# Kernel tuning notes

Measured on AMD Instinct MI355X. Metric: run time of the kernel, lower is better.

The kernel has to match this reference:

```python
import jax, jax.numpy as jnp
import numpy as np
import math

B, S, D = 4, 1024, 1024
H, DH = 16, 64
DFF = 4 * D
NEG = -1e9


def _layernorm(x, g, b, eps=1e-5):
    mu = jnp.mean(x, axis=-1, keepdims=True)
    var = jnp.var(x, axis=-1, keepdims=True)
    return (x - mu) * jax.lax.rsqrt(var + eps) * g + b


def setup_inputs() -> dict:
    key = jax.random.key(0)
    ks = jax.random.split(key, 12)
    inp = {
        "input": jax.random.normal(ks[0], (B, S, D), dtype=jnp.float32),
        # additive causal mask: 0 on/below diagonal, -1e9 above
        "causal_mask": jnp.where(
            jnp.tril(jnp.ones((S, S), dtype=bool)), 0.0, NEG
        ).astype(jnp.float32)[None, None],
        # additive padding mask: last 64 tokens of each sequence are padding
        "padding_mask": jnp.where(jnp.arange(S) < S - 64, 0.0, NEG)
        .astype(jnp.float32)[None, None, None, :]
        .repeat(B, axis=0),
        "ln1_g": jnp.ones((D,), jnp.float32), "ln1_b": jnp.zeros((D,), jnp.float32),
        "ln2_g": jnp.ones((D,), jnp.float32), "ln2_b": jnp.zeros((D,), jnp.float32),
        "ln3_g": jnp.ones((D,), jnp.float32), "ln3_b": jnp.zeros((D,), jnp.float32),
        "Wq": jax.random.normal(ks[1], (D, H * DH), jnp.float32) * 0.02,
        "bq": jnp.zeros((H * DH,), jnp.float32),
        "Wk": jax.random.normal(ks[2], (D, H * DH), jnp.float32) * 0.02,
        "bk": jnp.zeros((H * DH,), jnp.float32),
        "Wv": jax.random.normal(ks[3], (D, H * DH), jnp.float32) * 0.02,
        "bv": jnp.zeros((H * DH,), jnp.float32),
        "Wo": jax.random.normal(ks[4], (H * DH, D), jnp.float32) * 0.02,
        "bo": jnp.zeros((D,), jnp.float32),
        "W1": jax.random.normal(ks[5], (D, DFF), jnp.float32) * 0.02,
        "b1": jnp.zeros((DFF,), jnp.float32),
        "W2": jax.random.normal(ks[6], (DFF, D), jnp.float32) * 0.02,
        "b2": jnp.zeros((D,), jnp.float32),
    }
    return inp


def reference(input, causal_mask, padding_mask,
              ln1_g, ln1_b, ln2_g, ln2_b, ln3_g, ln3_b,
              Wq, bq, Wk, bk, Wv, bv, Wo, bo, W1, b1, W2, b2):
    x = _layernorm(input, ln1_g, ln1_b)
    b, s, _ = x.shape

    def heads(y):  # [b,s,H*DH] -> [b,H,s,DH]
        return y.reshape(b, s, H, DH).transpose(0, 2, 1, 3)

    q = heads(x @ Wq + bq)
    k = heads(x @ Wk + bk)
    v = heads(x @ Wv + bv)

    logits = jnp.einsum('bhqd,bhkd->bhqk', q, k) / math.sqrt(DH)
    logits = logits + causal_mask + padding_mask
    probs = jax.nn.softmax(logits, axis=-1)
    attn = jnp.einsum('bhqk,bhkd->bhqd', probs, v)
    attn = attn.transpose(0, 2, 1, 3).reshape(b, s, H * DH)  # b s (h d)
    attn_out = attn @ Wo + bo

    x = x + _layernorm(attn_out, ln2_g, ln2_b)
    h = _layernorm(x, ln3_g, ln3_b)
    x = x + (jax.nn.gelu(h @ W1 + b1, approximate=False) @ W2 + b2)
    return x
```

## Files before the change

### kernel.cpp

```cpp
#include <hip/hip_runtime.h>
#include <hip/hip_bf16.h>

typedef __hip_bfloat16 bf16;
typedef __bf16 bf16x8 __attribute__((ext_vector_type(8)));
typedef float f32x4 __attribute__((ext_vector_type(4)));

#define DEV __device__ __forceinline__

DEV int swz(int r, int k) { return r * 64 + (k ^ ((r & 7) << 3)); }

#define GLOAD_LDS16(gaddr, laddr)                                              \
  __builtin_amdgcn_global_load_lds(                                            \
      (const __attribute__((address_space(1))) void*)(gaddr),                  \
      (__attribute__((address_space(3))) void*)(laddr), 16, 0, 0)

__global__ void prep_kernel(
    const float* __restrict__ Wq, const float* __restrict__ Wk,
    const float* __restrict__ Wv, const float* __restrict__ Wo,
    const float* __restrict__ W1, const float* __restrict__ W2,
    const float* __restrict__ bq, const float* __restrict__ bk,
    const float* __restrict__ bv,
    bf16* __restrict__ WqkvT, bf16* __restrict__ WoT,
    bf16* __restrict__ W1T, bf16* __restrict__ W2T, float* __restrict__ bqkv) {
  int bid = blockIdx.x;
  if (bid >= 12288) {
    int i = (bid - 12288) * 256 + threadIdx.y * 32 + threadIdx.x;
    if (i < 3072)
      bqkv[i] = i < 1024 ? bq[i] : (i < 2048 ? bk[i - 1024] : bv[i - 2048]);
    return;
  }
  const float* src; bf16* dst; int K, N, tb;
  if (bid < 4096) {
    int wsel = bid >> 10;
    src = wsel == 0 ? Wq : wsel == 1 ? Wk : wsel == 2 ? Wv : Wo;
    dst = wsel < 3 ? WqkvT + (size_t)wsel * 1048576 : WoT;
    K = 1024; N = 1024; tb = bid & 1023;
  } else if (bid < 8192) {
    src = W1; dst = W1T; K = 1024; N = 4096; tb = bid - 4096;
  } else {
    src = W2; dst = W2T; K = 4096; N = 1024; tb = bid - 8192;
  }
  int ntx = N >> 5;
  int bx = (tb % ntx) * 32, by = (tb / ntx) * 32;
  __shared__ bf16 t[32][33];
  int tx = threadIdx.x, ty = threadIdx.y;
#pragma unroll
  for (int j = 0; j < 32; j += 8)
    t[ty + j][tx] = __float2bfloat16(src[(size_t)(by + ty + j) * N + bx + tx]);
  __syncthreads();
#pragma unroll
  for (int j = 0; j < 32; j += 8)
    dst[(size_t)(bx + ty + j) * K + by + tx] = t[tx][ty + j];
}

__global__ __launch_bounds__(256) void ln1_kernel(
    const float* __restrict__ in, const float* __restrict__ g, const float* __restrict__ b,
    float* __restrict__ xo, bf16* __restrict__ xb) {
  int row = blockIdx.x, tid = threadIdx.x;
  int lane = tid & 63, w = tid >> 6;
  float4 v = reinterpret_cast<const float4*>(in + (size_t)row * 1024)[tid];
  float s = v.x + v.y + v.z + v.w;
  float sq = v.x * v.x + v.y * v.y + v.z * v.z + v.w * v.w;
#pragma unroll
  for (int m = 32; m; m >>= 1) { s += __shfl_xor(s, m); sq += __shfl_xor(sq, m); }
  __shared__ float ss[4], qq[4];
  if (lane == 0) { ss[w] = s; qq[w] = sq; }
  __syncthreads();
  s = ss[0] + ss[1] + ss[2] + ss[3];
  sq = qq[0] + qq[1] + qq[2] + qq[3];
  float mu = s * (1.f / 1024.f);
  float rs = rsqrtf(sq * (1.f / 1024.f) - mu * mu + 1e-5f);
  float4 gg = reinterpret_cast<const float4*>(g)[tid];
  float4 bb = reinterpret_cast<const float4*>(b)[tid];
  float4 y;
  y.x = (v.x - mu) * rs * gg.x + bb.x;
  y.y = (v.y - mu) * rs * gg.y + bb.y;
  y.z = (v.z - mu) * rs * gg.z + bb.z;
  y.w = (v.w - mu) * rs * gg.w + bb.w;
  reinterpret_cast<float4*>(xo + (size_t)row * 1024)[tid] = y;
  union { bf16 h[4]; uint2 u; } pk;
  pk.h[0] = __float2bfloat16(y.x); pk.h[1] = __float2bfloat16(y.y);
  pk.h[2] = __float2bfloat16(y.z); pk.h[3] = __float2bfloat16(y.w);
  reinterpret_cast<uint2*>(xb + (size_t)row * 1024)[tid] = pk.u;
}

__global__ __launch_bounds__(256) void ln23_kernel(
    const float* __restrict__ x, const float* __restrict__ ao,
    const float* __restrict__ g2, const float* __restrict__ b2,
    const float* __restrict__ g3, const float* __restrict__ b3,
    float* __restrict__ x2o, bf16* __restrict__ hb) {
  int row = blockIdx.x, tid = threadIdx.x;
  int lane = tid & 63, w = tid >> 6;
  float4 a = reinterpret_cast<const float4*>(ao + (size_t)row * 1024)[tid];
  float s = a.x + a.y + a.z + a.w;
  float sq = a.x * a.x + a.y * a.y + a.z * a.z + a.w * a.w;
#pragma unroll
  for (int m = 32; m; m >>= 1) { s += __shfl_xor(s, m); sq += __shfl_xor(sq, m); }
  __shared__ float s1[4], q1[4], s2[4], q2[4];
  if (lane == 0) { s1[w] = s; q1[w] = sq; }
  __syncthreads();
  s = s1[0] + s1[1] + s1[2] + s1[3];
  sq = q1[0] + q1[1] + q1[2] + q1[3];
  float mu = s * (1.f / 1024.f);
  float rs = rsqrtf(sq * (1.f / 1024.f) - mu * mu + 1e-5f);
  float4 xr = reinterpret_cast<const float4*>(x + (size_t)row * 1024)[tid];
  float4 gg = reinterpret_cast<const float4*>(g2)[tid];
  float4 bb = reinterpret_cast<const float4*>(b2)[tid];
  float4 x2;
  x2.x = xr.x + (a.x - mu) * rs * gg.x + bb.x;
  x2.y = xr.y + (a.y - mu) * rs * gg.y + bb.y;
  x2.z = xr.z + (a.z - mu) * rs * gg.z + bb.z;
  x2.w = xr.w + (a.w - mu) * rs * gg.w + bb.w;
  reinterpret_cast<float4*>(x2o + (size_t)row * 1024)[tid] = x2;
  s = x2.x + x2.y + x2.z + x2.w;
  sq = x2.x * x2.x + x2.y * x2.y + x2.z * x2.z + x2.w * x2.w;
#pragma unroll
  for (int m = 32; m; m >>= 1) { s += __shfl_xor(s, m); sq += __shfl_xor(sq, m); }
  if (lane == 0) { s2[w] = s; q2[w] = sq; }
  __syncthreads();
  s = s2[0] + s2[1] + s2[2] + s2[3];
  sq = q2[0] + q2[1] + q2[2] + q2[3];
  mu = s * (1.f / 1024.f);
  rs = rsqrtf(sq * (1.f / 1024.f) - mu * mu + 1e-5f);
  gg = reinterpret_cast<const float4*>(g3)[tid];
  bb = reinterpret_cast<const float4*>(b3)[tid];
  union { bf16 h[4]; uint2 u; } pk;
  pk.h[0] = __float2bfloat16((x2.x - mu) * rs * gg.x + bb.x);
  pk.h[1] = __float2bfloat16((x2.y - mu) * rs * gg.y + bb.y);
  pk.h[2] = __float2bfloat16((x2.z - mu) * rs * gg.z + bb.z);
  pk.h[3] = __float2bfloat16((x2.w - mu) * rs * gg.w + bb.w);
  reinterpret_cast<uint2*>(hb + (size_t)row * 1024)[tid] = pk.u;
}

template <int BM, int BN, int WM, int WN, int MINW,
          bool GELU, bool RES, bool OUTBF, bool VSPLIT>
__global__ __launch_bounds__(WM * WN * 64, MINW) void gemm_db(
    const bf16* __restrict__ A, const bf16* __restrict__ BT,
    const float* __restrict__ bias, const float* __restrict__ res,
    float* __restrict__ outf, bf16* __restrict__ outb,
    bf16* __restrict__ kt, bf16* __restrict__ vt,
    int M, int N, int K) {
  constexpr int NW = WM * WN;
  constexpr int MT = BM / WM / 16, NT = BN / WN / 16;
  constexpr int ACH = BM / 8, BCH = BN / 8;
  constexpr int PW = (ACH + BCH) / NW;
  __shared__ __align__(16) bf16 As[2][BM * 64];
  __shared__ __align__(16) bf16 Bs[2][BN * 64];
  const int t = threadIdx.x, lane = t & 63, w = t >> 6;
  const int wr = w / WN, wc = w % WN;
  const int l15 = lane & 15, l4 = lane >> 4;
  const int gx = gridDim.x, nwg = gx * gridDim.y;
  int bid = blockIdx.y * gx + blockIdx.x;
  int sbid = (bid & 7) * (nwg >> 3) + (bid >> 3);
  const int m0 = (sbid / gx) * BM, n0 = (sbid % gx) * BN;
  const int lr = lane >> 3;
  const int scol = ((lane & 7) * 8) ^ (lr * 8);

  auto stage = [&](int buf, int kt_) {
    const int k0 = kt_ << 6;
#pragma unroll
    for (int i = 0; i < PW; ++i) {
      int c = w * PW + i;
      if (c < ACH) {
        GLOAD_LDS16(A + (size_t)(m0 + c * 8 + lr) * K + k0 + scol, &As[buf][c * 512]);
      } else {
        int c2 = c - ACH;
        GLOAD_LDS16(BT + (size_t)(n0 + c2 * 8 + lr) * K + k0 + scol, &Bs[buf][c2 * 512]);
      }
    }
  };

  f32x4 acc[MT][NT] = {};
  const int nk = K >> 6;
  stage(0, 0);
  __syncthreads();
  int cur = 0;
  for (int kk = 0; kk < nk; ++kk) {
    if (kk + 1 < nk) stage(cur ^ 1, kk + 1);
#pragma unroll
    for (int ks = 0; ks < 2; ++ks) {
      bf16x8 af[MT], bfr[NT];
#pragma unroll
      for (int m = 0; m < MT; ++m)
        af[m] = *reinterpret_cast<const bf16x8*>(
            &As[cur][swz(wr * (BM / WM) + m * 16 + l15, ks * 32 + l4 * 8)]);
#pragma unroll
      for (int n = 0; n < NT; ++n)
        bfr[n] = *reinterpret_cast<const bf16x8*>(
            &Bs[cur][swz(wc * (BN / WN) + n * 16 + l15, ks * 32 + l4 * 8)]);
      __builtin_amdgcn_s_setprio(1);
#pragma unroll
      for (int m = 0; m < MT; ++m)
#pragma unroll
        for (int n = 0; n < NT; ++n)
          acc[m][n] = __builtin_amdgcn_mfma_f32_16x16x32_bf16(af[m], bfr[n], acc[m][n], 0, 0, 0);
      __builtin_amdgcn_s_setprio(0);
    }
    __syncthreads();
    cur ^= 1;
  }

#pragma unroll
  for (int m = 0; m < MT; ++m) {
    int gr0 = m0 + wr * (BM / WM) + m * 16 + l4 * 4;
#pragma unroll
    for (int n = 0; n < NT; ++n) {
      int gc = n0 + wc * (BN / WN) + n * 16 + l15;
      float bv = bias[gc];
#pragma unroll
      for (int q = 0; q < 4; ++q) {
        int gr = gr0 + q;
        float v = acc[m][n][q] + bv;
        if constexpr (GELU) v = 0.5f * v * (1.f + erff(v * 0.70710678118654752f));
        if constexpr (RES) v += res[(size_t)gr * N + gc];
        if constexpr (VSPLIT) {
          int s = gr & 1023, bb = gr >> 10;
          if (gc < 1024) {
            outb[(size_t)gr * N + gc] = __float2bfloat16(v);
          } else if (gc < 2048) {
            int hd = gc - 1024, hh = hd >> 6, d = hd & 63;
            int ln = (s & 15) | (((d >> 3) & 3) << 4);
            kt[(((size_t)(bb * 16 + hh) * 64 + (s >> 4)) << 10) + (d >> 5) * 512 +
               ln * 8 + (d & 7)] = __float2bfloat16(v);
          } else {
            int hd = gc - 2048, hh = hd >> 6, d = hd & 63;
            int ln = (d & 15) | (((s >> 3) & 3) << 4);
            vt[(((size_t)(bb * 16 + hh) * 4 + (d >> 4)) << 14) + ((s >> 5) << 9) +
               ln * 8 + (s & 7)] = __float2bfloat16(v);
          }
        } else if constexpr (OUTBF) {
          outb[(size_t)gr * N + gc] = __float2bfloat16(v);
        } else {
          outf[(size_t)gr * N + gc] = v;
        }
      }
    }
  }
}

__global__ __launch_bounds__(256, 2) void attn_kernel(
    const bf16* __restrict__ qkv, const bf16* __restrict__ kt,
    const bf16* __restrict__ vt, bf16* __restrict__ o) {
  const int S = 1024, QS = 3072, HD = 1024;
  const bf16* qg = qkv;
  int bid = blockIdx.x;
  int xcd = bid & 7, j = bid >> 3;
  int grp = xcd * 8 + (j >> 3);
  int pr = j & 7;
  const int b = grp >> 4, h = grp & 15;
  const int t = threadIdx.x, lane = t & 63, w = t >> 6;
  const int l15 = lane & 15, l4 = lane >> 4;

  constexpr int PSTR = 72;
  __shared__ __align__(16) bf16 P[4][16 * PSTR];

  const int bh = b * 16 + h;
  const bf16* kbase = kt + ((size_t)bh << 16) + lane * 8;
  const bf16* vbase = vt + ((size_t)bh << 16) + lane * 8;

  bf16x8 kA[8], kB[8];
  auto loadK = [&](int kb, bf16x8* kf) {
#pragma unroll
    for (int cb = 0; cb < 4; ++cb)
#pragma unroll
      for (int ks = 0; ks < 2; ++ks)
        kf[cb * 2 + ks] = *reinterpret_cast<const bf16x8*>(
            kbase + (((kb >> 4) + cb) << 10) + (ks << 9));
  };

  auto run_strip = [&](int q0) {
    bf16x8 qf0, qf1;
    {
      const bf16* qp = qg + (size_t)(b * S + q0 + l15) * QS + h * 64 + l4 * 8;
      qf0 = *reinterpret_cast<const bf16x8*>(qp);
      qf1 = *reinterpret_cast<const bf16x8*>(qp + 32);
    }
    f32x4 acc[4] = {};
    float mrow = -1e30f, lrow = 0.f;
    const int kmaxa = q0 + 15, kmax = kmaxa < 959 ? kmaxa : 959;
    const int nt = (kmax >> 6) + 1;
    loadK(0, kA);

    for (int kt_ = 0; kt_ < nt; ++kt_) {
      const int kb = kt_ << 6;
      bf16x8* kf = (kt_ & 1) ? kB : kA;
      bf16x8* kn = (kt_ & 1) ? kA : kB;
      bf16x8 vf[8];
#pragma unroll
      for (int n = 0; n < 4; ++n)
#pragma unroll
        for (int ks = 0; ks < 2; ++ks)
          vf[n * 2 + ks] = *reinterpret_cast<const bf16x8*>(
              vbase + (n << 14) + (((kb >> 5) + ks) << 9));
      if (kt_ + 1 < nt) loadK(kb + 64, kn);

      f32x4 sc[4];
      __builtin_amdgcn_s_setprio(1);
#pragma unroll
      for (int cb = 0; cb < 4; ++cb) {
        f32x4 z = {};
        z = __builtin_amdgcn_mfma_f32_16x16x32_bf16(kf[cb * 2 + 0], qf0, z, 0, 0, 0);
        z = __builtin_amdgcn_mfma_f32_16x16x32_bf16(kf[cb * 2 + 1], qf1, z, 0, 0, 0);
        sc[cb] = z;
      }
      __builtin_amdgcn_s_setprio(0);

      const int q = q0 + l15;
      float p[16];
#pragma unroll
      for (int cb = 0; cb < 4; ++cb)
#pragma unroll
        for (int r = 0; r < 4; ++r) {
          int kgl = kb + cb * 16 + l4 * 4 + r;
          p[cb * 4 + r] = (kgl > q) ? -1e30f : sc[cb][r] * 0.125f;
        }
      float tm = p[0];
#pragma unroll
      for (int i = 1; i < 16; ++i) tm = fmaxf(tm, p[i]);
      tm = fmaxf(tm, __shfl_xor(tm, 16));
      tm = fmaxf(tm, __shfl_xor(tm, 32));
      bool defer = __all(tm <= mrow + 8.f);
      float mn = defer ? mrow : fmaxf(mrow, tm);
      float ps = 0.f;
#pragma unroll
      for (int i = 0; i < 16; ++i) { p[i] = __expf(p[i] - mn); ps += p[i]; }
      ps += __shfl_xor(ps, 16);
      ps += __shfl_xor(ps, 32);
      if (defer) {
        lrow += ps;
      } else {
        float al = __expf(mrow - mn);
        mrow = mn;
        lrow = lrow * al + ps;
#pragma unroll
        for (int n = 0; n < 4; ++n)
#pragma unroll
          for (int r = 0; r < 4; ++r) acc[n][r] *= al;
      }
#pragma unroll
      for (int cb = 0; cb < 4; ++cb) {
        union { bf16 h4[4]; uint2 u; } pk;
#pragma unroll
        for (int r = 0; r < 4; ++r) pk.h4[r] = __float2bfloat16(p[cb * 4 + r]);
        *reinterpret_cast<uint2*>(&P[w][l15 * PSTR + cb * 16 + l4 * 4]) = pk.u;
      }
      asm volatile("" ::: "memory");
      bf16x8 pb0 = *reinterpret_cast<const bf16x8*>(&P[w][l15 * PSTR + l4 * 8]);
      bf16x8 pb1 = *reinterpret_cast<const bf16x8*>(&P[w][l15 * PSTR + 32 + l4 * 8]);
      __builtin_amdgcn_s_setprio(1);
#pragma unroll
      for (int n = 0; n < 4; ++n) {
        acc[n] = __builtin_amdgcn_mfma_f32_16x16x32_bf16(vf[n * 2 + 0], pb0, acc[n], 0, 0, 0);
        acc[n] = __builtin_amdgcn_mfma_f32_16x16x32_bf16(vf[n * 2 + 1], pb1, acc[n], 0, 0, 0);
      }
      __builtin_amdgcn_s_setprio(0);
    }

    float inv = 1.f / lrow;
#pragma unroll
    for (int n = 0; n < 4; ++n) {
      union { bf16 h4[4]; uint2 u; } pk;
#pragma unroll
      for (int r = 0; r < 4; ++r) pk.h4[r] = __float2bfloat16(acc[n][r] * inv);
      *reinterpret_cast<uint2*>(&P[w][l15 * PSTR + n * 16 + l4 * 4]) = pk.u;
    }
    asm volatile("" ::: "memory");
    {
      int qq = lane >> 2, c = lane & 3;
#pragma unroll
      for (int i = 0; i < 2; ++i) {
        uint4 ov = *reinterpret_cast<const uint4*>(&P[w][qq * PSTR + c * 16 + i * 8]);
        *reinterpret_cast<uint4*>(
            o + (size_t)(b * S + q0 + qq) * HD + h * 64 + c * 16 + i * 8) = ov;
      }
    }
    asm volatile("" ::: "memory");
  };

  run_strip(pr * 64 + w * 16);
  run_strip((15 - pr) * 64 + w * 16);
}

extern "C" void kernel_launch(void* const* d_in, const int* in_sizes, int n_in,
                              void* d_out, int out_size, void* d_ws, size_t ws_size,
                              hipStream_t stream) {
  const float* input = (const float*)d_in[0];
  const float* ln1g = (const float*)d_in[3];
  const float* ln1b = (const float*)d_in[4];
  const float* ln2g = (const float*)d_in[5];
  const float* ln2b = (const float*)d_in[6];
  const float* ln3g = (const float*)d_in[7];
  const float* ln3b = (const float*)d_in[8];
  const float* Wq = (const float*)d_in[9];  const float* bq = (const float*)d_in[10];
  const float* Wk = (const float*)d_in[11]; const float* bk = (const float*)d_in[12];
  const float* Wv = (const float*)d_in[13]; const float* bv = (const float*)d_in[14];
  const float* Wo = (const float*)d_in[15]; const float* bo = (const float*)d_in[16];
  const float* W1 = (const float*)d_in[17]; const float* b1 = (const float*)d_in[18];
  const float* W2 = (const float*)d_in[19]; const float* b2 = (const float*)d_in[20];

  const int M = 4096, D = 1024, F = 4096;
  char* p = (char*)d_ws;
  size_t off = 0;
  auto nxt = [&](size_t n) { char* r = p + off; off += n; return r; };
  bf16* WqkvT = (bf16*)nxt((size_t)3 * D * D * 2);
  bf16* WoT = (bf16*)nxt((size_t)D * D * 2);
  bf16* W1T = (bf16*)nxt((size_t)F * D * 2);
  bf16* W2T = (bf16*)nxt((size_t)D * F * 2);
  float* bqkv = (float*)nxt(16384);
  float* xf  = (float*)nxt((size_t)M * D * 4);
  float* aof = (float*)nxt((size_t)M * D * 4);
  float* x2f = (float*)nxt((size_t)M * D * 4);
  bf16* xb = (bf16*)nxt((size_t)M * D * 2);
  bf16* qkv = (bf16*)nxt((size_t)M * 3 * D * 2);
  bf16* ktb = (bf16*)aof;
  bf16* vtb = (bf16*)((char*)aof + (size_t)8 * 1024 * 1024);
  bf16* gb = (bf16*)xf;
  bf16* ab = xb;
  bf16* hb = qkv;

  prep_kernel<<<12300, dim3(32, 8), 0, stream>>>(
      Wq, Wk, Wv, Wo, W1, W2, bq, bk, bv, WqkvT, WoT, W1T, W2T, bqkv);

  ln1_kernel<<<M, 256, 0, stream>>>(input, ln1g, ln1b, xf, xb);

  gemm_db<256, 256, 2, 4, 2, false, false, true, true>
      <<<dim3(12, 16), 512, 0, stream>>>(
      xb, WqkvT, bqkv, nullptr, nullptr, qkv, ktb, vtb, M, 3 * D, D);

  attn_kernel<<<512, 256, 0, stream>>>(qkv, ktb, vtb, ab);

  gemm_db<128, 64, 2, 2, 4, false, false, false, false>
      <<<dim3(16, 32), 256, 0, stream>>>(
      ab, WoT, bo, nullptr, aof, nullptr, nullptr, nullptr, M, D, D);

  ln23_kernel<<<M, 256, 0, stream>>>(xf, aof, ln2g, ln2b, ln3g, ln3b, x2f, hb);

  gemm_db<256, 256, 2, 4, 2, true, false, true, false>
      <<<dim3(16, 16), 512, 0, stream>>>(
      hb, W1T, b1, nullptr, nullptr, gb, nullptr, nullptr, M, F, D);
  gemm_db<128, 64, 2, 2, 4, false, true, false, false>
      <<<dim3(16, 32), 256, 0, stream>>>(
      gb, W2T, b2, x2f, (float*)d_out, nullptr, nullptr, nullptr, M, D, F);
}
```

Before: 221.6 us.

## Add phased GEMM kernel interleaving half-tile loads with MFMA for QKV and FFN1

Adds a 256x256 GEMM kernel that splits each 64-wide K tile into four 32-column half-stages (A and B, two K halves). It issues the async global-to-LDS loads for the next tile between four MFMA phases, using explicit vmcnt waits, barriers and s_setprio. The aim is to overlap memory traffic with matrix math at finer grain and to cut full-tile sync stalls in the QKV and W1 GEMMs. It also changes the LDS swizzle and the B-fragment reuse across M halves. The cost is more barriers and hand-tuned wait counts that must match the number of loads in flight.

```diff
diff --git a/kernel.cpp b/kernel.cpp
--- a/kernel.cpp
+++ b/kernel.cpp
@@ -132,13 +132,136 @@
   reinterpret_cast<uint2*>(hb + (size_t)row * 1024)[tid] = pk.u;
 }
 
+template <bool GELU, bool VSPLIT>
+__global__ __launch_bounds__(512, 1) void gemm_8ph(
+    const bf16* __restrict__ A, const bf16* __restrict__ BT,
+    const float* __restrict__ bias, bf16* __restrict__ outb,
+    bf16* __restrict__ kt, bf16* __restrict__ vt,
+    int M, int N, int K) {
+  __shared__ __align__(16) bf16 LDS[2][4][256 * 32];
+  const int t = threadIdx.x, lane = t & 63, w = t >> 6;
+  const int wr = w >> 2, wc = w & 3;
+  const int l15 = lane & 15, l4 = lane >> 4;
+  const int gx = gridDim.x, nwg = gx * gridDim.y;
+  int bid = blockIdx.y * gx + blockIdx.x;
+  int sbid = (bid & 7) * (nwg >> 3) + (bid >> 3);
+  const int m0 = (sbid / gx) * 256, n0 = (sbid % gx) * 256;
+  const int srow = lane >> 2;
+  const int scol8 = (((lane & 3) ^ ((lane >> 3) & 3)) << 3);
+  const int ldrd = l15 * 32 + ((l4 ^ ((l15 >> 1) & 3)) << 3);
+
+  auto stage_half = [&](int buf, int tile, int h) {
+    const bf16* P = (h & 1) ? BT : A;
+    const int rb = (h & 1) ? n0 : m0;
+    const int col = (tile << 6) + ((h >> 1) << 5) + scol8;
+#pragma unroll
+    for (int i = 0; i < 2; ++i) {
+      int c = w * 2 + i;
+      GLOAD_LDS16(P + (size_t)(rb + c * 16 + srow) * K + col, &LDS[buf][h][c * 512]);
+    }
+  };
+
+  f32x4 acc[8][4] = {};
+  bf16x8 bfr[4];
+
+  auto mfma_phase = [&](int cb, int ks, int mh, bool loadB) {
+    const bf16* Ah = &LDS[cb][ks * 2][0];
+    if (loadB) {
+      const bf16* Bh = &LDS[cb][ks * 2 + 1][0];
+#pragma unroll
+      for (int n = 0; n < 4; ++n)
+        bfr[n] = *reinterpret_cast<const bf16x8*>(Bh + wc * 2048 + n * 512 + ldrd);
+    }
+    bf16x8 af[4];
+#pragma unroll
+    for (int m = 0; m < 4; ++m)
+      af[m] = *reinterpret_cast<const bf16x8*>(Ah + wr * 4096 + mh * 2048 + m * 512 + ldrd);
+    __builtin_amdgcn_s_setprio(1);
+#pragma unroll
+    for (int m = 0; m < 4; ++m)
+#pragma unroll
+      for (int n = 0; n < 4; ++n)
+        acc[mh * 4 + m][n] =
+            __builtin_amdgcn_mfma_f32_16x16x32_bf16(af[m], bfr[n], acc[mh * 4 + m][n], 0, 0, 0);
+    __builtin_amdgcn_s_setprio(0);
+  };
+
+  const int nk = K >> 6;
+#pragma unroll
+  for (int h = 0; h < 4; ++h) stage_half(0, 0, h);
+
+  for (int tt = 0; tt < nk - 1; ++tt) {
+    const int cb = tt & 1;
+    asm volatile("s_waitcnt vmcnt(4)" ::: "memory");
+    asm volatile("s_barrier" ::: "memory");
+    stage_half(cb ^ 1, tt + 1, 0);
+    mfma_phase(cb, 0, 0, true);
+    asm volatile("s_barrier" ::: "memory");
+    stage_half(cb ^ 1, tt + 1, 1);
+    mfma_phase(cb, 0, 1, false);
+    asm volatile("s_waitcnt vmcnt(4)" ::: "memory");
+    asm volatile("s_barrier" ::: "memory");
+    stage_half(cb ^ 1, tt + 1, 2);
+    mfma_phase(cb, 1, 0, true);
+    asm volatile("s_barrier" ::: "memory");
+    stage_half(cb ^ 1, tt + 1, 3);
+    mfma_phase(cb, 1, 1, false);
+  }
+  {
+    const int cb = (nk - 1) & 1;
+    asm volatile("s_waitcnt vmcnt(4)" ::: "memory");
+    asm volatile("s_barrier" ::: "memory");
+    mfma_phase(cb, 0, 0, true);
+    asm volatile("s_barrier" ::: "memory");
+    mfma_phase(cb, 0, 1, false);
+    asm volatile("s_waitcnt vmcnt(0)" ::: "memory");
+    asm volatile("s_barrier" ::: "memory");
+    mfma_phase(cb, 1, 0, true);
+    asm volatile("s_barrier" ::: "memory");
+    mfma_phase(cb, 1, 1, false);
+  }
+
+#pragma unroll
+  for (int m = 0; m < 8; ++m) {
+    int gr0 = m0 + wr * 128 + m * 16 + l4 * 4;
+#pragma unroll
+    for (int n = 0; n < 4; ++n) {
+      int gc = n0 + wc * 64 + n * 16 + l15;
+      float bv = bias[gc];
+#pragma unroll
+      for (int q = 0; q < 4; ++q) {
+        int gr = gr0 + q;
+        float v = acc[m][n][q] + bv;
+        if constexpr (GELU) v = 0.5f * v * (1.f + erff(v * 0.70710678118654752f));
+        if constexpr (VSPLIT) {
+          int s = gr & 1023, bb = gr >> 10;
+          if (gc < 1024) {
+            outb[(size_t)gr * N + gc] = __float2bfloat16(v);
+          } else if (gc < 2048) {
+            int hd = gc - 1024, hh = hd >> 6, d = hd & 63;
+            int ln = (s & 15) | (((d >> 3) & 3) << 4);
+            kt[(((size_t)(bb * 16 + hh) * 64 + (s >> 4)) << 10) + (d >> 5) * 512 +
+               ln * 8 + (d & 7)] = __float2bfloat16(v);
+          } else {
+            int hd = gc - 2048, hh = hd >> 6, d = hd & 63;
+            int ln = (d & 15) | (((s >> 3) & 3) << 4);
+            vt[(((size_t)(bb * 16 + hh) * 4 + (d >> 4)) << 14) + ((s >> 5) << 9) +
+               ln * 8 + (s & 7)] = __float2bfloat16(v);
+          }
+        } else {
+          outb[(size_t)gr * N + gc] = __float2bfloat16(v);
+        }
+      }
+    }
+  }
+}
+
 template <int BM, int BN, int WM, int WN, int MINW,
-          bool GELU, bool RES, bool OUTBF, bool VSPLIT>
+          bool GELU, bool RES, bool OUTBF>
 __global__ __launch_bounds__(WM * WN * 64, MINW) void gemm_db(
     const bf16* __restrict__ A, const bf16* __restrict__ BT,
     const float* __restrict__ bias, const float* __restrict__ res,
     float* __restrict__ outf, bf16* __restrict__ outb,
-    bf16* __restrict__ kt, bf16* __restrict__ vt,
     int M, int N, int K) {
   constexpr int NW = WM * WN;
   constexpr int MT = BM / WM / 16, NT = BN / WN / 16;
@@ -213,26 +336,8 @@
         float v = acc[m][n][q] + bv;
         if constexpr (GELU) v = 0.5f * v * (1.f + erff(v * 0.70710678118654752f));
         if constexpr (RES) v += res[(size_t)gr * N + gc];
-        if constexpr (VSPLIT) {
-          int s = gr & 1023, bb = gr >> 10;
-          if (gc < 1024) {
-            outb[(size_t)gr * N + gc] = __float2bfloat16(v);
-          } else if (gc < 2048) {
-            int hd = gc - 1024, hh = hd >> 6, d = hd & 63;
-            int ln = (s & 15) | (((d >> 3) & 3) << 4);
-            kt[(((size_t)(bb * 16 + hh) * 64 + (s >> 4)) << 10) + (d >> 5) * 512 +
-               ln * 8 + (d & 7)] = __float2bfloat16(v);
-          } else {
-            int hd = gc - 2048, hh = hd >> 6, d = hd & 63;
-            int ln = (d & 15) | (((s >> 3) & 3) << 4);
-            vt[(((size_t)(bb * 16 + hh) * 4 + (d >> 4)) << 14) + ((s >> 5) << 9) +
-               ln * 8 + (s & 7)] = __float2bfloat16(v);
-          }
-        } else if constexpr (OUTBF) {
-          outb[(size_t)gr * N + gc] = __float2bfloat16(v);
-        } else {
-          outf[(size_t)gr * N + gc] = v;
-        }
+        if constexpr (OUTBF) outb[(size_t)gr * N + gc] = __float2bfloat16(v);
+        else                 outf[(size_t)gr * N + gc] = v;
       }
     }
   }
@@ -423,22 +528,20 @@
 
   ln1_kernel<<<M, 256, 0, stream>>>(input, ln1g, ln1b, xf, xb);
 
-  gemm_db<256, 256, 2, 4, 2, false, false, true, true>
-      <<<dim3(12, 16), 512, 0, stream>>>(
-      xb, WqkvT, bqkv, nullptr, nullptr, qkv, ktb, vtb, M, 3 * D, D);
+  gemm_8ph<false, true><<<dim3(12, 16), 512, 0, stream>>>(
+      xb, WqkvT, bqkv, qkv, ktb, vtb, M, 3 * D, D);
 
   attn_kernel<<<512, 256, 0, stream>>>(qkv, ktb, vtb, ab);
 
-  gemm_db<128, 64, 2, 2, 4, false, false, false, false>
+  gemm_db<128, 64, 2, 2, 4, false, false, false>
       <<<dim3(16, 32), 256, 0, stream>>>(
-      ab, WoT, bo, nullptr, aof, nullptr, nullptr, nullptr, M, D, D);
+      ab, WoT, bo, nullptr, aof, nullptr, M, D, D);
 
   ln23_kernel<<<M, 256, 0, stream>>>(xf, aof, ln2g, ln2b, ln3g, ln3b, x2f, hb);
 
-  gemm_db<256, 256, 2, 4, 2, true, false, true, false>
-      <<<dim3(16, 16), 512, 0, stream>>>(
-      hb, W1T, b1, nullptr, nullptr, gb, nullptr, nullptr, M, F, D);
-  gemm_db<128, 64, 2, 2, 4, false, true, false, false>
+  gemm_8ph<true, false><<<dim3(16, 16), 512, 0, stream>>>(
+      hb, W1T, b1, gb, nullptr, nullptr, M, F, D);
+  gemm_db<128, 64, 2, 2, 4, false, true, false>
       <<<dim3(16, 32), 256, 0, stream>>>(
-      gb, W2T, b2, x2f, (float*)d_out, nullptr, nullptr, nullptr, M, D, F);
-}
+      gb, W2T, b2, x2f, (float*)d_out, nullptr, M, D, F);
+}
```

New measurement: 222.8 us. Within noise of the previous version (+0.5%).

## Fuse LN1 into prep kernel, overlap FFN weight conversion with attention

Applied to the files above, without the earlier changes.

The LayerNorm-1 row work is merged into the weight-prep launch as extra blocks, and the W1/W2 transpose-to-bf16 conversion moves into the attention launch as extra blocks after the 512 attention blocks. The QKV GEMM tile changes from 256x256 to 256x192 so the grid grows from 12x16 to 16x16. The goal is fewer kernel launches, filling idle CUs during attention with the memory-bound weight conversion, and better CU coverage for the QKV GEMM. The risk is that the extra blocks in the attention kernel compete with it for memory bandwidth and add LDS per block, which could lower attention occupancy.

```diff
diff --git a/kernel.cpp b/kernel.cpp
--- a/kernel.cpp
+++ b/kernel.cpp
@@ -17,71 +17,61 @@
 __global__ void prep_kernel(
     const float* __restrict__ Wq, const float* __restrict__ Wk,
     const float* __restrict__ Wv, const float* __restrict__ Wo,
-    const float* __restrict__ W1, const float* __restrict__ W2,
     const float* __restrict__ bq, const float* __restrict__ bk,
     const float* __restrict__ bv,
-    bf16* __restrict__ WqkvT, bf16* __restrict__ WoT,
-    bf16* __restrict__ W1T, bf16* __restrict__ W2T, float* __restrict__ bqkv) {
+    bf16* __restrict__ WqkvT, bf16* __restrict__ WoT, float* __restrict__ bqkv,
+    const float* __restrict__ in, const float* __restrict__ g1,
+    const float* __restrict__ b1v, float* __restrict__ xo, bf16* __restrict__ xb) {
+  __shared__ bf16 t[32][33];
+  __shared__ float ss[4], qq[4];
   int bid = blockIdx.x;
-  if (bid >= 12288) {
-    int i = (bid - 12288) * 256 + threadIdx.y * 32 + threadIdx.x;
+  if (bid >= 4108) {
+    int row = bid - 4108, tid = threadIdx.y * 32 + threadIdx.x;
+    int lane = tid & 63, w = tid >> 6;
+    float4 v = reinterpret_cast<const float4*>(in + (size_t)row * 1024)[tid];
+    float s = v.x + v.y + v.z + v.w;
+    float sq = v.x * v.x + v.y * v.y + v.z * v.z + v.w * v.w;
+#pragma unroll
+    for (int m = 32; m; m >>= 1) { s += __shfl_xor(s, m); sq += __shfl_xor(sq, m); }
+    if (lane == 0) { ss[w] = s; qq[w] = sq; }
+    __syncthreads();
+    s = ss[0] + ss[1] + ss[2] + ss[3];
+    sq = qq[0] + qq[1] + qq[2] + qq[3];
+    float mu = s * (1.f / 1024.f);
+    float rs = rsqrtf(sq * (1.f / 1024.f) - mu * mu + 1e-5f);
+    float4 gg = reinterpret_cast<const float4*>(g1)[tid];
+    float4 bb = reinterpret_cast<const float4*>(b1v)[tid];
+    float4 y;
+    y.x = (v.x - mu) * rs * gg.x + bb.x;
+    y.y = (v.y - mu) * rs * gg.y + bb.y;
+    y.z = (v.z - mu) * rs * gg.z + bb.z;
+    y.w = (v.w - mu) * rs * gg.w + bb.w;
+    reinterpret_cast<float4*>(xo + (size_t)row * 1024)[tid] = y;
+    union { bf16 h[4]; uint2 u; } pk;
+    pk.h[0] = __float2bfloat16(y.x); pk.h[1] = __float2bfloat16(y.y);
+    pk.h[2] = __float2bfloat16(y.z); pk.h[3] = __float2bfloat16(y.w);
+    reinterpret_cast<uint2*>(xb + (size_t)row * 1024)[tid] = pk.u;
+    return;
+  }
+  if (bid >= 4096) {
+    int i = (bid - 4096) * 256 + threadIdx.y * 32 + threadIdx.x;
     if (i < 3072)
       bqkv[i] = i < 1024 ? bq[i] : (i < 2048 ? bk[i - 1024] : bv[i - 2048]);
     return;
   }
-  const float* src; bf16* dst; int K, N, tb;
-  if (bid < 4096) {
-    int wsel = bid >> 10;
-    src = wsel == 0 ? Wq : wsel == 1 ? Wk : wsel == 2 ? Wv : Wo;
-    dst = wsel < 3 ? WqkvT + (size_t)wsel * 1048576 : WoT;
-    K = 1024; N = 1024; tb = bid & 1023;
-  } else if (bid < 8192) {
-    src = W1; dst = W1T; K = 1024; N = 4096; tb = bid - 4096;
-  } else {
-    src = W2; dst = W2T; K = 4096; N = 1024; tb = bid - 8192;
-  }
-  int ntx = N >> 5;
-  int bx = (tb % ntx) * 32, by = (tb / ntx) * 32;
-  __shared__ bf16 t[32][33];
+  int wsel = bid >> 10;
+  const float* src = wsel == 0 ? Wq : wsel == 1 ? Wk : wsel == 2 ? Wv : Wo;
+  bf16* dst = wsel < 3 ? WqkvT + (size_t)wsel * 1048576 : WoT;
+  int tb = bid & 1023;
+  int bx = (tb & 31) * 32, by = (tb >> 5) * 32;
   int tx = threadIdx.x, ty = threadIdx.y;
 #pragma unroll
   for (int j = 0; j < 32; j += 8)
-    t[ty + j][tx] = __float2bfloat16(src[(size_t)(by + ty + j) * N + bx + tx]);
+    t[ty + j][tx] = __float2bfloat16(src[(size_t)(by + ty + j) * 1024 + bx + tx]);
   __syncthreads();
 #pragma unroll
   for (int j = 0; j < 32; j += 8)
-    dst[(size_t)(bx + ty + j) * K + by + tx] = t[tx][ty + j];
-}
-
-__global__ __launch_bounds__(256) void ln1_kernel(
-    const float* __restrict__ in, const float* __restrict__ g, const float* __restrict__ b,
-    float* __restrict__ xo, bf16* __restrict__ xb) {
-  int row = blockIdx.x, tid = threadIdx.x;
-  int lane = tid & 63, w = tid >> 6;
-  float4 v = reinterpret_cast<const float4*>(in + (size_t)row * 1024)[tid];
-  float s = v.x + v.y + v.z + v.w;
-  float sq = v.x * v.x + v.y * v.y + v.z * v.z + v.w * v.w;
-#pragma unroll
-  for (int m = 32; m; m >>= 1) { s += __shfl_xor(s, m); sq += __shfl_xor(sq, m); }
-  __shared__ float ss[4], qq[4];
-  if (lane == 0) { ss[w] = s; qq[w] = sq; }
-  __syncthreads();
-  s = ss[0] + ss[1] + ss[2] + ss[3];
-  sq = qq[0] + qq[1] + qq[2] + qq[3];
-  float mu = s * (1.f / 1024.f);
-  float rs = rsqrtf(sq * (1.f / 1024.f) - mu * mu + 1e-5f);
-  float4 gg = reinterpret_cast<const float4*>(g)[tid];
-  float4 bb = reinterpret_cast<const float4*>(b)[tid];
-  float4 y;
-  y.x = (v.x - mu) * rs * gg.x + bb.x;
-  y.y = (v.y - mu) * rs * gg.y + bb.y;
-  y.z = (v.z - mu) * rs * gg.z + bb.z;
-  y.w = (v.w - mu) * rs * gg.w + bb.w;
-  reinterpret_cast<float4*>(xo + (size_t)row * 1024)[tid] = y;
-  union { bf16 h[4]; uint2 u; } pk;
-  pk.h[0] = __float2bfloat16(y.x); pk.h[1] = __float2bfloat16(y.y);
-  pk.h[2] = __float2bfloat16(y.z); pk.h[3] = __float2bfloat16(y.w);
-  reinterpret_cast<uint2*>(xb + (size_t)row * 1024)[tid] = pk.u;
+    dst[(size_t)(bx + ty + j) * 1024 + by + tx] = t[tx][ty + j];
 }
 
 __global__ __launch_bounds__(256) void ln23_kernel(
@@ -240,20 +230,39 @@
 
 __global__ __launch_bounds__(256, 2) void attn_kernel(
     const bf16* __restrict__ qkv, const bf16* __restrict__ kt,
-    const bf16* __restrict__ vt, bf16* __restrict__ o) {
+    const bf16* __restrict__ vt, bf16* __restrict__ o,
+    const float* __restrict__ W1, const float* __restrict__ W2,
+    bf16* __restrict__ W1T, bf16* __restrict__ W2T) {
   const int S = 1024, QS = 3072, HD = 1024;
-  const bf16* qg = qkv;
+  constexpr int PSTR = 72;
+  __shared__ __align__(16) bf16 P[4][16 * PSTR];
+  __shared__ bf16 tt[32][33];
   int bid = blockIdx.x;
+  const int t = threadIdx.x, lane = t & 63, w = t >> 6;
+  if (bid >= 512) {
+    int b2 = bid - 512;
+    const float* src; bf16* dst; int K, N, tb;
+    if (b2 < 4096) { src = W1; dst = W1T; K = 1024; N = 4096; tb = b2; }
+    else           { src = W2; dst = W2T; K = 4096; N = 1024; tb = b2 - 4096; }
+    int ntx = N >> 5;
+    int bx = (tb % ntx) * 32, by = (tb / ntx) * 32;
+    int tx = t & 31, ty = t >> 5;
+#pragma unroll
+    for (int j = 0; j < 32; j += 8)
+      tt[ty + j][tx] = __float2bfloat16(src[(size_t)(by + ty + j) * N + bx + tx]);
+    __syncthreads();
+#pragma unroll
+    for (int j = 0; j < 32; j += 8)
+      dst[(size_t)(bx + ty + j) * K + by + tx] = tt[tx][ty + j];
+    return;
+  }
   int xcd = bid & 7, j = bid >> 3;
   int grp = xcd * 8 + (j >> 3);
   int pr = j & 7;
   const int b = grp >> 4, h = grp & 15;
-  const int t = threadIdx.x, lane = t & 63, w = t >> 6;
   const int l15 = lane & 15, l4 = lane >> 4;
 
-  constexpr int PSTR = 72;
-  __shared__ __align__(16) bf16 P[4][16 * PSTR];
-
+  const bf16* qg = qkv;
   const int bh = b * 16 + h;
   const bf16* kbase = kt + ((size_t)bh << 16) + lane * 8;
   const bf16* vbase = vt + ((size_t)bh << 16) + lane * 8;
@@ -418,16 +427,15 @@
   bf16* ab = xb;
   bf16* hb = qkv;
 
-  prep_kernel<<<12300, dim3(32, 8), 0, stream>>>(
-      Wq, Wk, Wv, Wo, W1, W2, bq, bk, bv, WqkvT, WoT, W1T, W2T, bqkv);
-
-  ln1_kernel<<<M, 256, 0, stream>>>(input, ln1g, ln1b, xf, xb);
-
-  gemm_db<256, 256, 2, 4, 2, false, false, true, true>
-      <<<dim3(12, 16), 512, 0, stream>>>(
+  prep_kernel<<<4108 + 4096, dim3(32, 8), 0, stream>>>(
+      Wq, Wk, Wv, Wo, bq, bk, bv, WqkvT, WoT, bqkv,
+      input, ln1g, ln1b, xf, xb);
+
+  gemm_db<256, 192, 2, 4, 1, false, false, true, true>
+      <<<dim3(16, 16), 512, 0, stream>>>(
       xb, WqkvT, bqkv, nullptr, nullptr, qkv, ktb, vtb, M, 3 * D, D);
 
-  attn_kernel<<<512, 256, 0, stream>>>(qkv, ktb, vtb, ab);
+  attn_kernel<<<512 + 8192, 256, 0, stream>>>(qkv, ktb, vtb, ab, W1, W2, W1T, W2T);
 
   gemm_db<128, 64, 2, 2, 4, false, false, false, false>
       <<<dim3(16, 32), 256, 0, stream>>>(
```

Measured after the change: 214.7 us. 3.1% less time.
